# Optimization experiments

Measured on AMD Instinct MI355X. Metric: run time of the kernel, lower is better.

## Reference

```python
import jax, jax.numpy as jnp
import numpy as np

C = 256

def _conv1x1(x, w, b):
    # x: [B,C,H,W], w: [O,I], b: [O]  (1x1 conv == pointwise GEMM over channels)
    return jnp.einsum('oi,bihw->bohw', w, x) + b[None, :, None, None]

def setup_inputs() -> dict:
    key = jax.random.key(0)
    ks = jax.random.split(key, 9)
    s = 1.0 / np.sqrt(C)
    x = jax.random.normal(ks[0], (16, C, 64, 64), dtype=jnp.float32)
    wf = jax.random.uniform(ks[1], (C, C), jnp.float32, -s, s)
    bf = jax.random.uniform(ks[2], (C,), jnp.float32, -s, s)
    wg = jax.random.uniform(ks[3], (C, C), jnp.float32, -s, s)
    bg = jax.random.uniform(ks[4], (C,), jnp.float32, -s, s)
    wh = jax.random.uniform(ks[5], (C, C), jnp.float32, -s, s)
    bh = jax.random.uniform(ks[6], (C,), jnp.float32, -s, s)
    wv = jax.random.uniform(ks[7], (C, C), jnp.float32, -s, s)
    bv = jax.random.uniform(ks[8], (C,), jnp.float32, -s, s)
    return {"x": x, "wf": wf, "bf": bf, "wg": wg, "bg": bg,
            "wh": wh, "bh": bh, "wv": wv, "bv": bv}

def reference(x, wf, bf, wg, bg, wh, bh, wv, bv):
    fx = _conv1x1(x, wf, bf)              # [B,C,H,W]
    gx = _conv1x1(x, wg, bg)              # [B,C,H,W]
    # scores: fx^T @ gx over spatial H -> [B,C,W,W]
    scores = jnp.einsum('bchw,bchv->bcwv', fx, gx)
    attn = jax.nn.softmax(scores, axis=-1)  # softmax over last W dim
    hx = _conv1x1(x, wh, bh)              # [B,C,H,W]
    out = jnp.einsum('bchw,bcwv->bchv', hx, attn)  # hx @ attn -> [B,C,H,W]
    return _conv1x1(out, wv, bv)
```

## Files before the change

### kernel.cpp

```cpp
#include <hip/hip_runtime.h>
#include <math.h>

#define CH  256
#define SPA 4096
#define BB  16
#define PLANE 16777216

typedef _Float16 f16x8 __attribute__((ext_vector_type(8)));
typedef _Float16 f16x4 __attribute__((ext_vector_type(4)));
typedef float    f32x4 __attribute__((ext_vector_type(4)));

__device__ __forceinline__ void gload16(const void* g, void* l) {
    __builtin_amdgcn_global_load_lds(
        (const __attribute__((address_space(1))) unsigned int*)g,
        (__attribute__((address_space(3))) unsigned int*)l, 16, 0, 0);
}

__global__ __launch_bounds__(256) void xpose_kernel(
    const float* __restrict__ src, _Float16* __restrict__ dst)
{
    __shared__ float T[64][65];
    const int t  = threadIdx.x;
    const int b  = blockIdx.x >> 8;
    const int st = (blockIdx.x >> 2) & 63;
    const int rt = blockIdx.x & 3;
    const int s0 = st << 6, r0 = rt << 6;

    #pragma unroll
    for (int p = 0; p < 4; ++p) {
        int k = (t >> 4) + (p << 4);
        float4 v = *(const float4*)(src + (((size_t)((b << 8) + r0 + k)) << 12)
                                        + s0 + ((t & 15) << 2));
        T[k][((t & 15) << 2) + 0] = v.x;
        T[k][((t & 15) << 2) + 1] = v.y;
        T[k][((t & 15) << 2) + 2] = v.z;
        T[k][((t & 15) << 2) + 3] = v.w;
    }
    __syncthreads();

    const int s  = t >> 2;
    const int kg = (t & 3) << 4;
    const size_t obase = (((size_t)((b << 12) + s0 + s)) << 8) + r0 + kg;

    f16x8 h0, h1;
    #pragma unroll
    for (int i = 0; i < 16; ++i) {
        _Float16 hv = (_Float16)T[kg + i][s];
        if (i < 8) h0[i] = hv; else h1[i - 8] = hv;
    }
    *(f16x8*)(dst + obase)     = h0;
    *(f16x8*)(dst + obase + 8) = h1;
}

__global__ __launch_bounds__(256) void cpose_kernel(
    const _Float16* __restrict__ src, _Float16* __restrict__ dst)
{
    __shared__ _Float16 T[64][68];
    const int t  = threadIdx.x;
    const int b  = blockIdx.x >> 8;
    const int st = (blockIdx.x >> 2) & 63;
    const int ct = blockIdx.x & 3;
    const int s0 = st << 6, c0 = ct << 6;

    #pragma unroll
    for (int p = 0; p < 4; ++p) {
        int fi = (p << 8) + t;
        int r = fi >> 4, s4 = (fi & 15) << 2;
        f16x4 v = *(const f16x4*)(src + (((size_t)((b << 8) + c0 + r)) << 12) + s0 + s4);
        *(f16x4*)&T[r][s4] = v;
    }
    __syncthreads();

    const int s  = t >> 2;
    const int cg = (t & 3) << 4;
    f16x8 h0, h1;
    #pragma unroll
    for (int i = 0; i < 16; ++i) {
        _Float16 hv = T[cg + i][s];
        if (i < 8) h0[i] = hv; else h1[i - 8] = hv;
    }
    const size_t obase = (((size_t)((b << 12) + s0 + s)) << 8) + c0 + cg;
    *(f16x8*)(dst + obase)     = h0;
    *(f16x8*)(dst + obase + 8) = h1;
}

__global__ __launch_bounds__(256) void wcvt_kernel(
    const float* __restrict__ w0, const float* __restrict__ w1,
    const float* __restrict__ w2, const float* __restrict__ w3,
    _Float16* __restrict__ dst)
{
    const int idx = blockIdx.x * 256 + threadIdx.x;
    dst[idx]             = (_Float16)w0[idx];
    dst[65536 + idx]     = (_Float16)w1[idx];
    dst[131072 + idx]    = (_Float16)w2[idx];
    dst[196608 + idx]    = (_Float16)w3[idx];
}

template<int NM, bool OUTF16>
__global__ __launch_bounds__(256) void gemm16_kernel(
    const _Float16* __restrict__ xT, const _Float16* __restrict__ wc,
    const float* __restrict__ bias0, const float* __restrict__ bias1,
    const float* __restrict__ bias2, void* __restrict__ outp)
{
    __shared__ _Float16 S[8192];
    _Float16* sA = S;
    _Float16* sB = S + 4096;

    int m, r_;
    if (NM == 3) { m = blockIdx.x % 3; r_ = blockIdx.x / 3; }
    else         { m = 0;              r_ = blockIdx.x; }
    const _Float16* wp = wc + m * 65536;
    const float* bias = (m == 0) ? bias0 : ((m == 1) ? bias1 : bias2);

    const int tid = threadIdx.x;
    const int w = tid >> 6, lane = tid & 63, quad = lane >> 4, li = lane & 15;
    const int wx = w & 1, wy = w >> 1;
    const int ot    = r_ & 1;
    const int stile = (r_ >> 1) & 31;
    const int b     = r_ >> 6;
    const int s0 = stile << 7, o0 = ot << 7;

    f32x4 acc[4][4];
    #pragma unroll
    for (int t2 = 0; t2 < 4; ++t2)
        #pragma unroll
        for (int u = 0; u < 4; ++u) acc[t2][u] = (f32x4){0.f, 0.f, 0.f, 0.f};

    const int rr = lane >> 2, cc = (lane & 3) << 3;

    for (int kb = 0; kb < CH; kb += 32) {
        __syncthreads();
        #pragma unroll
        for (int j = 0; j < 32; j += 16) {
            const int r = (w << 5) + j + rr;
            const size_t ga = (((size_t)((b << 12) + s0 + r)) << 8) + kb + cc;
            const size_t gb = ((size_t)(o0 + r) << 8) + kb + cc;
            const int lo_ = ((w << 5) + j) * 32 + lane * 8;
            gload16(xT + ga, sA + lo_);
            gload16(wp + gb, sB + lo_);
        }
        __syncthreads();

        f16x8 a[4], bfr[4];
        #pragma unroll
        for (int t2 = 0; t2 < 4; ++t2) {
            a[t2]   = *(const f16x8*)(sA + ((wy << 6) + (t2 << 4) + li) * 32 + (quad << 3));
            bfr[t2] = *(const f16x8*)(sB + ((wx << 6) + (t2 << 4) + li) * 32 + (quad << 3));
        }
        #pragma unroll
        for (int t2 = 0; t2 < 4; ++t2)
            #pragma unroll
            for (int u = 0; u < 4; ++u)
                acc[t2][u] = __builtin_amdgcn_mfma_f32_16x16x32_f16(a[t2], bfr[u], acc[t2][u], 0, 0, 0);
    }

    #pragma unroll
    for (int u = 0; u < 4; ++u) {
        const int o = o0 + (wx << 6) + (u << 4) + li;
        const float bz = bias[o];
        #pragma unroll
        for (int t2 = 0; t2 < 4; ++t2) {
            const int s = s0 + (wy << 6) + (t2 << 4) + (quad << 2);
            const size_t off = (((size_t)((b << 8) + o)) << 12) + s;
            f32x4 v = acc[t2][u];
            if (OUTF16) {
                _Float16* ob = (_Float16*)outp + (size_t)m * PLANE;
                f16x4 pv;
                pv[0] = (_Float16)(v[0] + bz); pv[1] = (_Float16)(v[1] + bz);
                pv[2] = (_Float16)(v[2] + bz); pv[3] = (_Float16)(v[3] + bz);
                *(f16x4*)(ob + off) = pv;
            } else {
                float* of = (float*)outp;
                float4 pv = {v[0] + bz, v[1] + bz, v[2] + bz, v[3] + bz};
                *(float4*)(of + off) = pv;
            }
        }
    }
}

__global__ __launch_bounds__(256) void attn_mfma_kernel(
    const _Float16* __restrict__ fx, const _Float16* __restrict__ gx,
    const _Float16* __restrict__ hx, _Float16* __restrict__ ob)
{
    __shared__ _Float16 L[23040];
    const int FT = 0, GT = 4608, HM = 9216;
    const int FR = 13824, GR = 18432;
    const int PT = 13824;

    const int t = threadIdx.x;
    const int wave = t >> 6, lane = t & 63, q = lane >> 4, li = lane & 15;
    const int bc = blockIdx.x;
    const _Float16* Fp = fx + (size_t)bc * SPA;
    const _Float16* Gp = gx + (size_t)bc * SPA;
    const _Float16* Hp = hx + (size_t)bc * SPA;
    _Float16* Op = ob + (size_t)bc * SPA;

    #pragma unroll
    for (int p = 0; p < 2; ++p) {
        int ci = t + (p << 8);
        int h = ci >> 3, w8 = (ci & 7) << 3;
        *(f16x8*)&L[FR + h * 72 + w8] = *(const f16x8*)(Fp + h * 64 + w8);
        *(f16x8*)&L[GR + h * 72 + w8] = *(const f16x8*)(Gp + h * 64 + w8);
        *(f16x8*)&L[HM + h * 72 + w8] = *(const f16x8*)(Hp + h * 64 + w8);
    }
    __syncthreads();

    {
        const int src = (wave < 2) ? FR : GR;
        const int dst = (wave < 2) ? FT : GT;
        const int mtb = (wave & 1) << 1;
        f16x8 id0, id1;
        #pragma unroll
        for (int j = 0; j < 8; ++j) {
            id0[j] = (_Float16)(((q << 3) + j == li)      ? 1.0f : 0.0f);
            id1[j] = (_Float16)(((q << 3) + j == li + 16) ? 1.0f : 0.0f);
        }
        #pragma unroll
        for (int mi = 0; mi < 2; ++mi) {
            const int mt = mtb + mi;
            f16x8 a0 = *(const f16x8*)&L[src + (mt * 16 + li) * 72 + (q << 3)];
            f16x8 a1 = *(const f16x8*)&L[src + (mt * 16 + li) * 72 + 32 + (q << 3)];
            #pragma unroll
            for (int nt = 0; nt < 4; ++nt) {
                f32x4 d = {0.f, 0.f, 0.f, 0.f};
                d = __builtin_amdgcn_mfma_f32_16x16x32_f16(
                        (nt < 2) ? a0 : a1, (nt & 1) ? id1 : id0, d, 0, 0, 0);
                f16x4 e;
                e[0] = (_Float16)d[0]; e[1] = (_Float16)d[1];
                e[2] = (_Float16)d[2]; e[3] = (_Float16)d[3];
                *(f16x4*)&L[dst + (nt * 16 + li) * 72 + mt * 16 + (q << 2)] = e;
            }
        }
    }
    __syncthreads();

    {
        f16x8 a0 = *(const f16x8*)&L[FT + (wave * 16 + li) * 72 + (q << 3)];
        f16x8 a1 = *(const f16x8*)&L[FT + (wave * 16 + li) * 72 + 32 + (q << 3)];
        f32x4 s_[4];
        #pragma unroll
        for (int nt = 0; nt < 4; ++nt) {
            f16x8 b0 = *(const f16x8*)&L[GT + (nt * 16 + li) * 72 + (q << 3)];
            f16x8 b1 = *(const f16x8*)&L[GT + (nt * 16 + li) * 72 + 32 + (q << 3)];
            f32x4 acc = {0.f, 0.f, 0.f, 0.f};
            acc = __builtin_amdgcn_mfma_f32_16x16x32_f16(a0, b0, acc, 0, 0, 0);
            acc = __builtin_amdgcn_mfma_f32_16x16x32_f16(a1, b1, acc, 0, 0, 0);
            s_[nt] = acc;
        }
        float mx[4], sm[4];
        #pragma unroll
        for (int r = 0; r < 4; ++r) {
            float m0 = fmaxf(fmaxf(s_[0][r], s_[1][r]), fmaxf(s_[2][r], s_[3][r]));
            m0 = fmaxf(m0, __shfl_xor(m0, 1));
            m0 = fmaxf(m0, __shfl_xor(m0, 2));
            m0 = fmaxf(m0, __shfl_xor(m0, 4));
            m0 = fmaxf(m0, __shfl_xor(m0, 8));
            mx[r] = m0;
        }
        #pragma unroll
        for (int nt = 0; nt < 4; ++nt)
            #pragma unroll
            for (int r = 0; r < 4; ++r)
                s_[nt][r] = __expf(s_[nt][r] - mx[r]);
        #pragma unroll
        for (int r = 0; r < 4; ++r) {
            float s0 = (s_[0][r] + s_[1][r]) + (s_[2][r] + s_[3][r]);
            s0 += __shfl_xor(s0, 1);
            s0 += __shfl_xor(s0, 2);
            s0 += __shfl_xor(s0, 4);
            s0 += __shfl_xor(s0, 8);
            sm[r] = 1.f / s0;
        }
        #pragma unroll
        for (int nt = 0; nt < 4; ++nt) {
            const int v  = nt * 16 + li;
            const int sw = ((v >> 3) & 7) << 3;
            #pragma unroll
            for (int r = 0; r < 4; ++r) {
                const int w = wave * 16 + (q << 2) + r;
                L[PT + v * 72 + (w ^ sw)] = (_Float16)(s_[nt][r] * sm[r]);
            }
        }
    }
    __syncthreads();

    {
        f16x8 a0 = *(const f16x8*)&L[HM + (wave * 16 + li) * 72 + (q << 3)];
        f16x8 a1 = *(const f16x8*)&L[HM + (wave * 16 + li) * 72 + 32 + (q << 3)];
        #pragma unroll
        for (int nt = 0; nt < 4; ++nt) {
            const int v  = nt * 16 + li;
            const int sw = ((v >> 3) & 7) << 3;
            f16x8 b0 = *(const f16x8*)&L[PT + v * 72 + ((q << 3) ^ sw)];
            f16x8 b1 = *(const f16x8*)&L[PT + v * 72 + ((32 + (q << 3)) ^ sw)];
            f32x4 acc = {0.f, 0.f, 0.f, 0.f};
            acc = __builtin_amdgcn_mfma_f32_16x16x32_f16(a0, b0, acc, 0, 0, 0);
            acc = __builtin_amdgcn_mfma_f32_16x16x32_f16(a1, b1, acc, 0, 0, 0);
            #pragma unroll
            for (int r = 0; r < 4; ++r)
                Op[(wave * 16 + (q << 2) + r) * 64 + v] = (_Float16)acc[r];
        }
    }
}

extern "C" void kernel_launch(void* const* d_in, const int* in_sizes, int n_in,
                              void* d_out, int out_size, void* d_ws, size_t ws_size,
                              hipStream_t stream)
{
    const float* x  = (const float*)d_in[0];
    const float* wf = (const float*)d_in[1];
    const float* bf = (const float*)d_in[2];
    const float* wg = (const float*)d_in[3];
    const float* bg = (const float*)d_in[4];
    const float* wh = (const float*)d_in[5];
    const float* bh = (const float*)d_in[6];
    const float* wv = (const float*)d_in[7];
    const float* bv = (const float*)d_in[8];

    char* base = (char*)d_ws;
    const size_t MB = 1ull << 20;
    _Float16* xT  = (_Float16*)base;
    _Float16* fxb = (_Float16*)(base + 32 * MB);
    _Float16* gxb = (_Float16*)(base + 64 * MB);
    _Float16* hxb = (_Float16*)(base + 96 * MB);
    _Float16* ob  = (_Float16*)(base + 128 * MB);
    _Float16* obT = (_Float16*)base;
    _Float16* wc  = (_Float16*)(base + 160 * MB);

    dim3 blk(256);
    xpose_kernel<<<4096, blk, 0, stream>>>(x, xT);
    wcvt_kernel<<<256, blk, 0, stream>>>(wf, wg, wh, wv, wc);

    gemm16_kernel<3, true><<<dim3(3072), blk, 0, stream>>>(
        xT, wc, bf, bg, bh, fxb);

    attn_mfma_kernel<<<4096, blk, 0, stream>>>(fxb, gxb, hxb, ob);

    cpose_kernel<<<4096, blk, 0, stream>>>(ob, obT);

    gemm16_kernel<1, false><<<dim3(1024), blk, 0, stream>>>(
        obT, wc + 196608, bv, bv, bv, d_out);
}
```

Baseline: 256.1 us.

## Fuse f/g/h projection GEMMs into one kernel sharing the x tile

Replaces the three-way split projection GEMM (one weight matrix per block) with a single kernel in which each block loads one 128-spatial x 32-channel tile of x into LDS and multiplies it against 64 output channels of all three weight matrices. The shared x tile is read once for f, g and h instead of three times, which cuts global and LDS traffic for the activation. The price is three times the accumulator registers per thread (24 MFMA accumulators), which may lower occupancy. The grid changes from 3072 to 2048 blocks. The output planes are now laid out contiguously, with gx and hx derived as offsets from fx.

```diff
diff --git a/kernel.cpp b/kernel.cpp
--- a/kernel.cpp
+++ b/kernel.cpp
@@ -96,25 +96,103 @@
     dst[196608 + idx]    = (_Float16)w3[idx];
 }
 
-template<int NM, bool OUTF16>
-__global__ __launch_bounds__(256) void gemm16_kernel(
+__global__ __launch_bounds__(256) void gemm_fgh_kernel(
     const _Float16* __restrict__ xT, const _Float16* __restrict__ wc,
     const float* __restrict__ bias0, const float* __restrict__ bias1,
-    const float* __restrict__ bias2, void* __restrict__ outp)
+    const float* __restrict__ bias2, _Float16* __restrict__ outp)
+{
+    __shared__ _Float16 S[10240];
+    _Float16* sA = S;
+
+    const int tid = threadIdx.x;
+    const int w = tid >> 6, lane = tid & 63, q = lane >> 4, li = lane & 15;
+    const int r_ = blockIdx.x;
+    const int ot    = r_ & 3;
+    const int stile = (r_ >> 2) & 31;
+    const int b     = r_ >> 7;
+    const int s0 = stile << 7, o0 = ot << 6;
+
+    const float* biases[3] = {bias0, bias1, bias2};
+
+    f32x4 acc[3][4][2];
+    #pragma unroll
+    for (int m = 0; m < 3; ++m)
+        #pragma unroll
+        for (int t2 = 0; t2 < 4; ++t2)
+            #pragma unroll
+            for (int u = 0; u < 2; ++u) acc[m][t2][u] = (f32x4){0.f, 0.f, 0.f, 0.f};
+
+    const int rr = tid >> 2;
+    const int cc = (tid & 3) << 3;
+
+    const int n0 = (w & 1) << 5;
+    const int m0 = (w >> 1) << 6;
+
+    for (int kb = 0; kb < CH; kb += 32) {
+        __syncthreads();
+        {
+            const size_t ga = (((size_t)((b << 12) + s0 + rr)) << 8) + kb + cc;
+            gload16(xT + ga, sA + tid * 8);
+            gload16(xT + ga + (64ull << 8), sA + 2048 + tid * 8);
+            #pragma unroll
+            for (int m = 0; m < 3; ++m) {
+                const size_t gb = (((size_t)(o0 + rr)) << 8) + m * 65536 + kb + cc;
+                gload16(wc + gb, S + 4096 + m * 2048 + tid * 8);
+            }
+        }
+        __syncthreads();
+
+        f16x8 a[4];
+        #pragma unroll
+        for (int t2 = 0; t2 < 4; ++t2)
+            a[t2] = *(const f16x8*)(sA + (m0 + (t2 << 4) + li) * 32 + (q << 3));
+
+        #pragma unroll
+        for (int m = 0; m < 3; ++m) {
+            const _Float16* sB = S + 4096 + m * 2048;
+            f16x8 b0 = *(const f16x8*)(sB + (n0 + li) * 32 + (q << 3));
+            f16x8 b1 = *(const f16x8*)(sB + (n0 + 16 + li) * 32 + (q << 3));
+            #pragma unroll
+            for (int t2 = 0; t2 < 4; ++t2) {
+                acc[m][t2][0] = __builtin_amdgcn_mfma_f32_16x16x32_f16(a[t2], b0, acc[m][t2][0], 0, 0, 0);
+                acc[m][t2][1] = __builtin_amdgcn_mfma_f32_16x16x32_f16(a[t2], b1, acc[m][t2][1], 0, 0, 0);
+            }
+        }
+    }
+
+    #pragma unroll
+    for (int m = 0; m < 3; ++m) {
+        _Float16* ob = outp + (size_t)m * PLANE;
+        #pragma unroll
+        for (int u = 0; u < 2; ++u) {
+            const int o = o0 + n0 + (u << 4) + li;
+            const float bz = biases[m][o];
+            #pragma unroll
+            for (int t2 = 0; t2 < 4; ++t2) {
+                const int s = s0 + m0 + (t2 << 4) + (q << 2);
+                const size_t off = (((size_t)((b << 8) + o)) << 12) + s;
+                f32x4 v = acc[m][t2][u];
+                f16x4 pv;
+                pv[0] = (_Float16)(v[0] + bz); pv[1] = (_Float16)(v[1] + bz);
+                pv[2] = (_Float16)(v[2] + bz); pv[3] = (_Float16)(v[3] + bz);
+                *(f16x4*)(ob + off) = pv;
+            }
+        }
+    }
+}
+
+__global__ __launch_bounds__(256) void gemm16_kernel(
+    const _Float16* __restrict__ xT, const _Float16* __restrict__ wp,
+    const float* __restrict__ bias, float* __restrict__ outp)
 {
     __shared__ _Float16 S[8192];
     _Float16* sA = S;
     _Float16* sB = S + 4096;
 
-    int m, r_;
-    if (NM == 3) { m = blockIdx.x % 3; r_ = blockIdx.x / 3; }
-    else         { m = 0;              r_ = blockIdx.x; }
-    const _Float16* wp = wc + m * 65536;
-    const float* bias = (m == 0) ? bias0 : ((m == 1) ? bias1 : bias2);
-
     const int tid = threadIdx.x;
     const int w = tid >> 6, lane = tid & 63, quad = lane >> 4, li = lane & 15;
     const int wx = w & 1, wy = w >> 1;
+    const int r_ = blockIdx.x;
     const int ot    = r_ & 1;
     const int stile = (r_ >> 1) & 31;
     const int b     = r_ >> 6;
@@ -163,17 +241,8 @@
             const int s = s0 + (wy << 6) + (t2 << 4) + (quad << 2);
             const size_t off = (((size_t)((b << 8) + o)) << 12) + s;
             f32x4 v = acc[t2][u];
-            if (OUTF16) {
-                _Float16* ob = (_Float16*)outp + (size_t)m * PLANE;
-                f16x4 pv;
-                pv[0] = (_Float16)(v[0] + bz); pv[1] = (_Float16)(v[1] + bz);
-                pv[2] = (_Float16)(v[2] + bz); pv[3] = (_Float16)(v[3] + bz);
-                *(f16x4*)(ob + off) = pv;
-            } else {
-                float* of = (float*)outp;
-                float4 pv = {v[0] + bz, v[1] + bz, v[2] + bz, v[3] + bz};
-                *(float4*)(of + off) = pv;
-            }
+            float4 pv = {v[0] + bz, v[1] + bz, v[2] + bz, v[3] + bz};
+            *(float4*)(outp + off) = pv;
         }
     }
 }
@@ -321,23 +390,22 @@
     const size_t MB = 1ull << 20;
     _Float16* xT  = (_Float16*)base;
     _Float16* fxb = (_Float16*)(base + 32 * MB);
-    _Float16* gxb = (_Float16*)(base + 64 * MB);
-    _Float16* hxb = (_Float16*)(base + 96 * MB);
     _Float16* ob  = (_Float16*)(base + 128 * MB);
     _Float16* obT = (_Float16*)base;
     _Float16* wc  = (_Float16*)(base + 160 * MB);
 
+    _Float16* gxb = fxb + PLANE;
+    _Float16* hxb = gxb + PLANE;
+
     dim3 blk(256);
     xpose_kernel<<<4096, blk, 0, stream>>>(x, xT);
     wcvt_kernel<<<256, blk, 0, stream>>>(wf, wg, wh, wv, wc);
 
-    gemm16_kernel<3, true><<<dim3(3072), blk, 0, stream>>>(
-        xT, wc, bf, bg, bh, fxb);
+    gemm_fgh_kernel<<<2048, blk, 0, stream>>>(xT, wc, bf, bg, bh, fxb);
 
     attn_mfma_kernel<<<4096, blk, 0, stream>>>(fxb, gxb, hxb, ob);
 
     cpose_kernel<<<4096, blk, 0, stream>>>(ob, obT);
 
-    gemm16_kernel<1, false><<<dim3(1024), blk, 0, stream>>>(
-        obT, wc + 196608, bv, bv, bv, d_out);
-}
+    gemm16_kernel<<<1024, blk, 0, stream>>>(obT, wc + 196608, bv, (float*)d_out);
+}
```

After: 249.5 us. -2.6%, faster.
